# Performance work log

Measured on AMD Instinct MI355X. Metric: run time of the kernel, lower is better.

Reference implementation:

```python
import jax, jax.numpy as jnp
import numpy as np

DIM = 768
HEADS = 12
HID = 3072  # mlp_ratio * dim
BATCH = 8
FRAMES = 16
GRID = 14
NTOK = GRID * GRID
LN_EPS = 1e-5
EPS = 1e-6


def setup_inputs() -> dict:
    key = jax.random.key(0)
    ks = jax.random.split(key, 8)
    w = lambda k, shape: jax.random.normal(k, shape, jnp.float32) * 0.02
    return {
        "x": jax.random.normal(ks[0], (BATCH * FRAMES, NTOK, DIM), jnp.float32),
        "ln1_w": jnp.ones((DIM,), jnp.float32),
        "ln1_b": jnp.zeros((DIM,), jnp.float32),
        "qkv_w": w(ks[1], (3 * DIM, DIM)),
        "proj_w": w(ks[2], (DIM, DIM)),
        "proj_b": jnp.zeros((DIM,), jnp.float32),
        "ln2_w": jnp.ones((DIM,), jnp.float32),
        "ln2_b": jnp.zeros((DIM,), jnp.float32),
        "fc1_w": w(ks[3], (HID, DIM)),
        "fc1_b": jnp.zeros((HID,), jnp.float32),
        "dw_w": w(ks[4], (HID, 1, 3, 3)),
        "dw_b": jnp.zeros((HID,), jnp.float32),
        "fc2_w": w(ks[5], (DIM, HID)),
        "fc2_b": jnp.zeros((DIM,), jnp.float32),
        "H": GRID,
        "W": GRID,
        "num_frames": FRAMES,
    }


def _layernorm(x, w, b):
    mu = jnp.mean(x, axis=-1, keepdims=True)
    var = jnp.mean(jnp.square(x - mu), axis=-1, keepdims=True)
    return (x - mu) * jax.lax.rsqrt(var + LN_EPS) * w + b


def _joint_ts_attention(xn, qkv_w, proj_w, proj_b, num_frames):
    # xn: (b*f, n, c)
    Bt, n, C = xn.shape
    h = HEADS
    e = C // h
    scale = e ** (-0.5)
    qkv = jnp.einsum('bnc,dc->bnd', xn, qkv_w).reshape(Bt, n, 3, h, e)
    q, k, v = qkv[:, :, 0], qkv[:, :, 1], qkv[:, :, 2]
    # ReLU feature map + scale offset
    q_ = jax.nn.relu(q) + scale
    k_ = jax.nn.relu(k) + scale
    b = Bt // num_frames
    m = num_frames * n  # joint time-space sequence length
    q_ = q_.reshape(b, m, h, e)
    k_ = k_.reshape(b, m, h, e)
    v_ = v.reshape(b, m, h, e)
    # kv_: (b, h, e, e)
    kv = jnp.einsum('bnhe,bnhd->bhed', k_, v_)
    k_sum = jnp.sum(k_, axis=1)  # (b, h, e)
    z = 1.0 / (jnp.einsum('bnhe,bhe->bnh', q_, k_sum) + EPS)  # (b, m, h)
    out = jnp.einsum('bnhe,bhed->bnhd', q_, kv) * z[..., None]  # (b, m, h, e)
    out = out.reshape(Bt, n, C)
    return jnp.einsum('bnc,dc->bnd', out, proj_w) + proj_b


def _dwconv(x, w, b, H, W):
    # x: (B, N, C) -> NCHW depthwise 3x3, pad 1
    Bn, n, c = x.shape
    xi = jnp.transpose(x, (0, 2, 1)).reshape(Bn, c, H, W)
    y = jax.lax.conv_general_dilated(
        xi, w, window_strides=(1, 1), padding=((1, 1), (1, 1)),
        dimension_numbers=('NCHW', 'OIHW', 'NCHW'), feature_group_count=c)
    y = y + b[None, :, None, None]
    return jnp.transpose(y.reshape(Bn, c, n), (0, 2, 1))


def reference(x, ln1_w, ln1_b, qkv_w, proj_w, proj_b, ln2_w, ln2_b,
              fc1_w, fc1_b, dw_w, dw_b, fc2_w, fc2_b, H, W, num_frames):
    # x = x + attn(norm1(x), num_frames)
    x = x + _joint_ts_attention(_layernorm(x, ln1_w, ln1_b), qkv_w, proj_w, proj_b, num_frames)
    # x = x + mlp(norm2(x), H, W)
    xn = _layernorm(x, ln2_w, ln2_b)
    hdn = jnp.einsum('bnc,hc->bnh', xn, fc1_w) + fc1_b
    hdn = _dwconv(hdn, dw_w, dw_b, H, W)
    hdn = jax.nn.gelu(hdn, approximate=False)
    out = jnp.einsum('bnh,ch->bnc', hdn, fc2_w) + fc2_b
    return x + out
```

## Files before the change

### kernel.cpp

```cpp
#include <hip/hip_runtime.h>

typedef unsigned short u16;
typedef unsigned int u32;

typedef __bf16 bf16x8 __attribute__((ext_vector_type(8)));
typedef float f32x4 __attribute__((ext_vector_type(4)));

#define DIM 768
#define HID 3072
#define NTOK 196
#define BT 128
#define NTOKENS (BT * NTOK)
#define MJ 3136
#define HEADS 12

#define SZ_WB   ((size_t)(2304*768 + 768*768 + 3072*768 + 768*3072) * 2)
#define SZ_XN   ((size_t)NTOKENS * DIM * 2)
#define SZ_QKV  ((size_t)NTOKENS * 2304 * 2)
#define SZ_X2   ((size_t)NTOKENS * DIM * 4)
#define SZ_HDN  ((size_t)NTOKENS * HID * 2)
#define SZ_KV   ((size_t)96 * 4096 * 4)
#define SZ_KS   ((size_t)96 * 64 * 4)
#define WS_NEED (SZ_WB + SZ_XN + SZ_QKV + SZ_X2 + SZ_HDN + SZ_KV + SZ_KS)

static void* g_buf = nullptr;

__device__ __forceinline__ float b2f(u16 u) {
  union { u32 i; float f; } x; x.i = ((u32)u) << 16; return x.f;
}
__device__ __forceinline__ u16 f2b(float f) {
  u32 x = __float_as_uint(f);
  return (u16)((x + 0x7fffu + ((x >> 16) & 1u)) >> 16);
}

__device__ __forceinline__ void gload_lds16(const u16* g, u16* l) {
  __builtin_amdgcn_global_load_lds(
      (const __attribute__((address_space(1))) u32*)g,
      (__attribute__((address_space(3))) u32*)l, 16, 0, 0);
}

__global__ __launch_bounds__(256) void cvt_f32_bf16(const float* __restrict__ in,
    u16* __restrict__ out, int n4)
{
  int i = blockIdx.x * 256 + threadIdx.x;
  if (i < n4) {
    float4 f = ((const float4*)in)[i];
    ushort4 r;
    r.x = f2b(f.x); r.y = f2b(f.y); r.z = f2b(f.z); r.w = f2b(f.w);
    ((ushort4*)out)[i] = r;
  }
}

__global__ __launch_bounds__(256) void zero_f32(float* __restrict__ p, int n) {
  int i = blockIdx.x * 256 + threadIdx.x;
  if (i < n) p[i] = 0.0f;
}

__global__ __launch_bounds__(256) void ln_kernel(const float* __restrict__ xin,
    const float* __restrict__ w, const float* __restrict__ b, u16* __restrict__ out)
{
  const int token = blockIdx.x * 4 + (threadIdx.x >> 6);
  const int lane = threadIdx.x & 63;
  float v[12];
  const float* x = xin + (size_t)token * DIM;
#pragma unroll
  for (int c = 0; c < 3; ++c) {
    float4 f = *(const float4*)(x + c * 256 + lane * 4);
    v[c*4+0] = f.x; v[c*4+1] = f.y; v[c*4+2] = f.z; v[c*4+3] = f.w;
  }
  float s = 0.f, sq = 0.f;
#pragma unroll
  for (int i = 0; i < 12; ++i) { s += v[i]; sq += v[i] * v[i]; }
#pragma unroll
  for (int off = 32; off > 0; off >>= 1) {
    s += __shfl_xor(s, off, 64);
    sq += __shfl_xor(sq, off, 64);
  }
  const float mean = s * (1.0f / 768.0f);
  const float var = sq * (1.0f / 768.0f) - mean * mean;
  const float rstd = rsqrtf(var + 1e-5f);
  u16* o = out + (size_t)token * DIM;
#pragma unroll
  for (int c = 0; c < 3; ++c) {
    float4 wv = *(const float4*)(w + c * 256 + lane * 4);
    float4 bv = *(const float4*)(b + c * 256 + lane * 4);
    ushort4 r;
    r.x = f2b((v[c*4+0] - mean) * rstd * wv.x + bv.x);
    r.y = f2b((v[c*4+1] - mean) * rstd * wv.y + bv.y);
    r.z = f2b((v[c*4+2] - mean) * rstd * wv.z + bv.z);
    r.w = f2b((v[c*4+3] - mean) * rstd * wv.w + bv.w);
    *(ushort4*)(o + c * 256 + lane * 4) = r;
  }
}

template<int MODE, int NXT, int NN, int KK>
__global__ __launch_bounds__(512, 2) void gemm8(
    const u16* __restrict__ A, const u16* __restrict__ W,
    const float* __restrict__ bias, const float* __restrict__ res,
    void* __restrict__ out)
{
  extern __shared__ char smem[];
  u16* As = (u16*)smem;
  u16* Bs = (u16*)(smem + 65536);

  const int t = threadIdx.x;
  const int l = t & 63;
  const int w = t >> 6;
  const int wm = w >> 2;
  const int wn = w & 3;

  constexpr int TOTAL = 98 * NXT;
  constexpr int Q8 = TOTAL >> 3;
  constexpr int R8 = TOTAL & 7;
  const int orig = blockIdx.x;
  const int xcd = orig & 7;
  const int idx = orig >> 3;
  const int wg = (xcd < R8) ? (xcd * (Q8 + 1) + idx)
                            : (R8 * (Q8 + 1) + (xcd - R8) * Q8 + idx);
  const int m0 = (wg / NXT) * 256;
  const int n0 = (wg % NXT) * 256;

  const int srow = w * 16 + (l >> 3);
  const int scol = ((l & 7) ^ (l >> 3)) * 8;
  const u16* gA = A + (size_t)(m0 + srow) * KK + scol;
  const u16* gB = W + (size_t)(n0 + srow) * KK + scol;
  u16* lA = As + w * 1024;
  u16* lB = Bs + w * 1024;

#define STAGE_A(bb, h, kt) do { \
    const u16* g_ = gA + (size_t)(h) * 128 * KK + (size_t)(kt) * 64; \
    u16* l_ = lA + (bb) * 16384 + (h) * 8192; \
    gload_lds16(g_, l_); \
    gload_lds16(g_ + (size_t)8 * KK, l_ + 512); } while (0)
#define STAGE_B(bb, h, kt) do { \
    const u16* g_ = gB + (size_t)(h) * 128 * KK + (size_t)(kt) * 64; \
    u16* l_ = lB + (bb) * 16384 + (h) * 8192; \
    gload_lds16(g_, l_); \
    gload_lds16(g_ + (size_t)8 * KK, l_ + 512); } while (0)

  const int lm = l & 15;
  const int qq = l >> 4;
  const int acol = (qq << 4) ^ ((l & 7) << 4);
  const int abase = (wm * 128 + lm) * 128 + acol;
  const int bbase = (wn * 64 + lm) * 128 + acol;

  f32x4 acc[8][4];
#pragma unroll
  for (int mi = 0; mi < 8; ++mi)
#pragma unroll
    for (int ni = 0; ni < 4; ++ni) acc[mi][ni] = (f32x4){0.f, 0.f, 0.f, 0.f};

  constexpr int NT = KK / 64;

  STAGE_A(0, 0, 0); STAGE_A(0, 1, 0); STAGE_B(0, 0, 0); STAGE_B(0, 1, 0);
  STAGE_A(1, 0, 1);
  asm volatile("s_waitcnt vmcnt(2)" ::: "memory");
  __builtin_amdgcn_s_barrier();

  for (int ti = 0; ti < NT; ++ti) {
    const int cb = ti & 1, nb = cb ^ 1;
    const char* Ac = (const char*)As + cb * 32768;
    const char* Bc = (const char*)Bs + cb * 32768;
    bf16x8 am[4][2], b01[2][2], b23[2][2];

#pragma unroll
    for (int mi = 0; mi < 4; ++mi) {
      const int off = abase + mi * 2048;
      am[mi][0] = *(const bf16x8*)(Ac + off);
      am[mi][1] = *(const bf16x8*)(Ac + (off ^ 64));
    }
#pragma unroll
    for (int ni = 0; ni < 2; ++ni) {
      const int off = bbase + ni * 2048;
      b01[ni][0] = *(const bf16x8*)(Bc + off);
      b01[ni][1] = *(const bf16x8*)(Bc + (off ^ 64));
    }
    if (ti + 1 < NT) STAGE_A(nb, 1, ti + 1);
    asm volatile("" ::: "memory");
    __builtin_amdgcn_s_barrier();
    asm volatile("s_waitcnt lgkmcnt(0)" ::: "memory");
    __builtin_amdgcn_s_setprio(1);
#pragma unroll
    for (int mi = 0; mi < 4; ++mi)
#pragma unroll
      for (int ni = 0; ni < 2; ++ni) {
        acc[mi][ni] = __builtin_amdgcn_mfma_f32_16x16x32_bf16(am[mi][0], b01[ni][0], acc[mi][ni], 0, 0, 0);
        acc[mi][ni] = __builtin_amdgcn_mfma_f32_16x16x32_bf16(am[mi][1], b01[ni][1], acc[mi][ni], 0, 0, 0);
      }
    __builtin_amdgcn_s_setprio(0);
    asm volatile("" ::: "memory");
    __builtin_amdgcn_s_barrier();

#pragma unroll
    for (int ni = 0; ni < 2; ++ni) {
      const int off = bbase + (ni + 2) * 2048;
      b23[ni][0] = *(const bf16x8*)(Bc + off);
      b23[ni][1] = *(const bf16x8*)(Bc + (off ^ 64));
    }
    if (ti + 1 < NT) STAGE_B(nb, 0, ti + 1);
    asm volatile("" ::: "memory");
    __builtin_amdgcn_s_barrier();
    asm volatile("s_waitcnt lgkmcnt(0)" ::: "memory");
    __builtin_amdgcn_s_setprio(1);
#pragma unroll
    for (int mi = 0; mi < 4; ++mi)
#pragma unroll
      for (int ni = 0; ni < 2; ++ni) {
        acc[mi][ni + 2] = __builtin_amdgcn_mfma_f32_16x16x32_bf16(am[mi][0], b23[ni][0], acc[mi][ni + 2], 0, 0, 0);
        acc[mi][ni + 2] = __builtin_amdgcn_mfma_f32_16x16x32_bf16(am[mi][1], b23[ni][1], acc[mi][ni + 2], 0, 0, 0);
      }
    __builtin_amdgcn_s_setprio(0);
    asm volatile("" ::: "memory");
    __builtin_amdgcn_s_barrier();

#pragma unroll
    for (int mi = 0; mi < 4; ++mi) {
      const int off = abase + 8192 + mi * 2048;
      am[mi][0] = *(const bf16x8*)(Ac + off);
      am[mi][1] = *(const bf16x8*)(Ac + (off ^ 64));
    }
    if (ti + 1 < NT) STAGE_B(nb, 1, ti + 1);
    asm volatile("" ::: "memory");
    __builtin_amdgcn_s_barrier();
    asm volatile("s_waitcnt lgkmcnt(0)" ::: "memory");
    __builtin_amdgcn_s_setprio(1);
#pragma unroll
    for (int mi = 0; mi < 4; ++mi)
#pragma unroll
      for (int ni = 0; ni < 2; ++ni) {
        acc[mi + 4][ni + 2] = __builtin_amdgcn_mfma_f32_16x16x32_bf16(am[mi][0], b23[ni][0], acc[mi + 4][ni + 2], 0, 0, 0);
        acc[mi + 4][ni + 2] = __builtin_amdgcn_mfma_f32_16x16x32_bf16(am[mi][1], b23[ni][1], acc[mi + 4][ni + 2], 0, 0, 0);
      }
    __builtin_amdgcn_s_setprio(0);
    asm volatile("" ::: "memory");
    __builtin_amdgcn_s_barrier();

    if (ti + 2 < NT) {
      STAGE_A(cb, 0, ti + 2);
      asm volatile("s_waitcnt vmcnt(2)" ::: "memory");
    } else {
      asm volatile("s_waitcnt vmcnt(0)" ::: "memory");
    }
    __builtin_amdgcn_s_barrier();
    __builtin_amdgcn_s_setprio(1);
#pragma unroll
    for (int mi = 0; mi < 4; ++mi)
#pragma unroll
      for (int ni = 0; ni < 2; ++ni) {
        acc[mi + 4][ni] = __builtin_amdgcn_mfma_f32_16x16x32_bf16(am[mi][0], b01[ni][0], acc[mi + 4][ni], 0, 0, 0);
        acc[mi + 4][ni] = __builtin_amdgcn_mfma_f32_16x16x32_bf16(am[mi][1], b01[ni][1], acc[mi + 4][ni], 0, 0, 0);
      }
    __builtin_amdgcn_s_setprio(0);
    asm volatile("" ::: "memory");
    __builtin_amdgcn_s_barrier();
  }
#undef STAGE_A
#undef STAGE_B

#pragma unroll
  for (int mi = 0; mi < 8; ++mi) {
    const int rbase = m0 + wm * 128 + mi * 16 + qq * 4;
#pragma unroll
    for (int ni = 0; ni < 4; ++ni) {
      const int col = n0 + wn * 64 + ni * 16 + lm;
      float bv = 0.f;
      if (MODE != 0) bv = bias[col];
#pragma unroll
      for (int r = 0; r < 4; ++r) {
        float v = acc[mi][ni][r];
        const size_t idxo = (size_t)(rbase + r) * NN + col;
        if (MODE == 0) {
          if (col < 1536) v = fmaxf(v, 0.0f) + 0.125f;
          ((u16*)out)[idxo] = f2b(v);
        } else if (MODE == 1) {
          ((float*)out)[idxo] = v + bv + res[idxo];
        } else if (MODE == 2) {
          ((u16*)out)[idxo] = f2b(v + bv);
        } else {
          ((float*)out)[idxo] = v + bv + res[idxo];
        }
      }
    }
  }
}

__global__ __launch_bounds__(256) void kv_reduce(const u16* __restrict__ qkv,
    float* __restrict__ kv, float* __restrict__ ksum)
{
  const int bh = blockIdx.x;
  const int s = blockIdx.y;
  const int b = bh / 12, h = bh % 12;
  __shared__ __align__(16) u16 ks[64 * 64];
  __shared__ __align__(16) u16 vs[64 * 64];
  const int t = threadIdx.x;
  const int e = t & 63;
  const int dg = (t >> 6) * 16;

  float acc[16];
#pragma unroll
  for (int j = 0; j < 16; ++j) acc[j] = 0.f;
  float ksacc = 0.f;

  for (int ch = s; ch < 49; ch += 8) {
    const size_t tokbase = (size_t)b * MJ + ch * 64;
    __syncthreads();
#pragma unroll
    for (int i = 0; i < 2; ++i) {
      int c = t + i * 256;
      int row = c >> 3, eo = (c & 7) * 8;
      const u16* base = qkv + (tokbase + row) * 2304 + h * 64 + eo;
      *(uint4*)&ks[row * 64 + eo] = *(const uint4*)(base + 768);
      *(uint4*)&vs[row * 64 + eo] = *(const uint4*)(base + 1536);
    }
    __syncthreads();
    for (int m = 0; m < 64; ++m) {
      float kf = b2f(ks[m * 64 + e]);
      ksacc += kf;
      bf16x8 v0 = *(const bf16x8*)&vs[m * 64 + dg];
      bf16x8 v1 = *(const bf16x8*)&vs[m * 64 + dg + 8];
#pragma unroll
      for (int j = 0; j < 8; ++j) {
        acc[j]     += kf * (float)v0[j];
        acc[j + 8] += kf * (float)v1[j];
      }
    }
  }
  float* dst = kv + (size_t)bh * 4096 + e * 64 + dg;
#pragma unroll
  for (int j = 0; j < 16; ++j) atomicAdd(&dst[j], acc[j]);
  if (dg == 0) atomicAdd(&ksum[bh * 64 + e], ksacc);
}

__global__ __launch_bounds__(256) void attn_out(const u16* __restrict__ qkv,
    const float* __restrict__ kv, const float* __restrict__ ksum,
    u16* __restrict__ outp)
{
  const int chunk = blockIdx.x;
  const int h = blockIdx.y;
  const int b = blockIdx.z;
  __shared__ float kvs[4096];
  __shared__ float kss[64];
  __shared__ float qs[4096];
  const int t = threadIdx.x;
  const float* kvsrc = kv + (size_t)(b * 12 + h) * 4096;
  for (int i = t; i < 1024; i += 256)
    ((float4*)kvs)[i] = ((const float4*)kvsrc)[i];
  if (t < 64) kss[t] = ksum[(b * 12 + h) * 64 + t];
  __syncthreads();
  const int wv = t >> 6, lane = t & 63;
  float* qw = &qs[wv * 1024];
  const size_t tok0 = (size_t)b * MJ + chunk * 64 + wv * 16;
#pragma unroll
  for (int i = 0; i < 16; ++i) {
    float q = b2f(qkv[(tok0 + i) * 2304 + h * 64 + lane]);
    float pd = q * kss[lane];
#pragma unroll
    for (int off = 32; off > 0; off >>= 1) pd += __shfl_xor(pd, off, 64);
    qw[i * 64 + lane] = q * (1.0f / (pd + 1e-6f));
  }
  float o[16];
#pragma unroll
  for (int i = 0; i < 16; ++i) o[i] = 0.f;
  for (int e = 0; e < 64; ++e) {
    const float kvc = kvs[e * 64 + lane];
#pragma unroll
    for (int i = 0; i < 16; ++i) o[i] += qw[i * 64 + e] * kvc;
  }
#pragma unroll
  for (int i = 0; i < 16; ++i)
    outp[(tok0 + i) * 768 + h * 64 + lane] = f2b(o[i]);
}

__global__ __launch_bounds__(256) void dwconv_gelu(u16* __restrict__ hdn,
    const float* __restrict__ w, const float* __restrict__ bias)
{
  __shared__ u16 pl[196 * 64];
  const int cb = blockIdx.x;
  const int fr = blockIdx.y;
  const int t = threadIdx.x;
  const int c0 = cb * 64;
  u16* base = hdn + (size_t)fr * 196 * HID + c0;
  for (int i = 0; i < 49; ++i) {
    int idx = i * 256 + t;
    int p = idx >> 6, c = idx & 63;
    pl[idx] = base[(size_t)p * HID + c];
  }
  __syncthreads();
  const int c = t & 63;
  const int pg = t >> 6;
  float wr[9];
#pragma unroll
  for (int k = 0; k < 9; ++k) wr[k] = w[(c0 + c) * 9 + k];
  const float bv = bias[c0 + c];
  for (int j = 0; j < 49; ++j) {
    const int p = pg + j * 4;
    const int py = p / 14, px = p % 14;
    float a = bv;
#pragma unroll
    for (int ky = 0; ky < 3; ++ky) {
      int yy = py + ky - 1;
      if (yy < 0 || yy > 13) continue;
#pragma unroll
      for (int kx = 0; kx < 3; ++kx) {
        int xx = px + kx - 1;
        if (xx < 0 || xx > 13) continue;
        a += wr[ky * 3 + kx] * b2f(pl[(yy * 14 + xx) * 64 + c]);
      }
    }
    float g = 0.5f * a * (1.0f + erff(a * 0.70710678118654752f));
    base[(size_t)p * HID + c] = f2b(g);
  }
}

static void set_gemm_attrs() {
  (void)hipFuncSetAttribute(reinterpret_cast<const void*>(&gemm8<0, 9, 2304, 768>),
                            hipFuncAttributeMaxDynamicSharedMemorySize, 131072);
  (void)hipFuncSetAttribute(reinterpret_cast<const void*>(&gemm8<1, 3, 768, 768>),
                            hipFuncAttributeMaxDynamicSharedMemorySize, 131072);
  (void)hipFuncSetAttribute(reinterpret_cast<const void*>(&gemm8<2, 12, 3072, 768>),
                            hipFuncAttributeMaxDynamicSharedMemorySize, 131072);
  (void)hipFuncSetAttribute(reinterpret_cast<const void*>(&gemm8<3, 3, 768, 3072>),
                            hipFuncAttributeMaxDynamicSharedMemorySize, 131072);
}
struct WsInit {
  WsInit() {
    (void)hipMalloc(&g_buf, WS_NEED);
    set_gemm_attrs();
  }
};
static WsInit g_wsinit;

extern "C" void kernel_launch(void* const* d_in, const int* in_sizes, int n_in,
                              void* d_out, int out_size, void* d_ws, size_t ws_size,
                              hipStream_t stream)
{
  (void)in_sizes; (void)n_in; (void)out_size;
  static bool attrs_once = [] { set_gemm_attrs(); return true; }();
  (void)attrs_once;

  const float* x     = (const float*)d_in[0];
  const float* ln1w  = (const float*)d_in[1];
  const float* ln1b  = (const float*)d_in[2];
  const float* qkvw  = (const float*)d_in[3];
  const float* projw = (const float*)d_in[4];
  const float* projb = (const float*)d_in[5];
  const float* ln2w  = (const float*)d_in[6];
  const float* ln2b  = (const float*)d_in[7];
  const float* fc1w  = (const float*)d_in[8];
  const float* fc1b  = (const float*)d_in[9];
  const float* dww   = (const float*)d_in[10];
  const float* dwb   = (const float*)d_in[11];
  const float* fc2w  = (const float*)d_in[12];
  const float* fc2b  = (const float*)d_in[13];

  char* p = (ws_size >= WS_NEED) ? (char*)d_ws : (char*)g_buf;
  u16* WQKV  = (u16*)p;   p += (size_t)2304 * 768 * 2;
  u16* WPROJ = (u16*)p;   p += (size_t)768 * 768 * 2;
  u16* WFC1  = (u16*)p;   p += (size_t)3072 * 768 * 2;
  u16* WFC2  = (u16*)p;   p += (size_t)768 * 3072 * 2;
  u16* XN    = (u16*)p;   p += SZ_XN;
  u16* QKV   = (u16*)p;   p += SZ_QKV;
  float* X2  = (float*)p; p += SZ_X2;
  u16* HDN   = (u16*)p;   p += SZ_HDN;
  float* KV  = (float*)p; p += SZ_KV;
  float* KS  = (float*)p; p += SZ_KS;

  cvt_f32_bf16<<<(2304*768/4 + 255)/256, 256, 0, stream>>>(qkvw, WQKV, 2304*768/4);
  cvt_f32_bf16<<<(768*768/4 + 255)/256, 256, 0, stream>>>(projw, WPROJ, 768*768/4);
  cvt_f32_bf16<<<(3072*768/4 + 255)/256, 256, 0, stream>>>(fc1w, WFC1, 3072*768/4);
  cvt_f32_bf16<<<(768*3072/4 + 255)/256, 256, 0, stream>>>(fc2w, WFC2, 768*3072/4);

  const int nz = 96 * 4096 + 96 * 64;
  zero_f32<<<(nz + 255) / 256, 256, 0, stream>>>(KV, nz);
  ln_kernel<<<NTOKENS / 4, 256, 0, stream>>>(x, ln1w, ln1b, XN);
  gemm8<0, 9, 2304, 768><<<98 * 9, 512, 131072, stream>>>(XN, WQKV, nullptr, nullptr, QKV);
  kv_reduce<<<dim3(96, 8), 256, 0, stream>>>(QKV, KV, KS);
  attn_out<<<dim3(49, 12, 8), 256, 0, stream>>>(QKV, KV, KS, XN);
  gemm8<1, 3, 768, 768><<<98 * 3, 512, 131072, stream>>>(XN, WPROJ, projb, x, X2);
  ln_kernel<<<NTOKENS / 4, 256, 0, stream>>>(X2, ln2w, ln2b, QKV);
  gemm8<2, 12, 3072, 768><<<98 * 12, 512, 131072, stream>>>(QKV, WFC1, fc1b, nullptr, HDN);
  dwconv_gelu<<<dim3(48, 128), 256, 0, stream>>>(HDN, dww, dwb);
  gemm8<3, 3, 768, 3072><<<98 * 3, 512, 131072, stream>>>(HDN, WFC2, fc2b, X2, (float*)d_out);
}
```

Measured before the change: 1.114 ms.

## Reorder GEMM prefetch stages and vectorize depthwise conv with wider channel tiles

The GEMM main loop now issues both halves of the next A tile together, two iterations ahead, and spreads the B-tile prefetches over the first two compute phases, with the vmcnt waits adjusted to match. This is meant to issue global-to-LDS loads earlier and hide more latency. The dwconv+GELU kernel now covers 128 channels per block and loads with 16-byte vector reads into a padded LDS tile. Each thread computes 4 channels with ushort4 LDS reads and stores, which cuts the number of scalar 2-byte global accesses and halves the grid.

```diff
diff --git a/kernel.cpp b/kernel.cpp
--- a/kernel.cpp
+++ b/kernel.cpp
@@ -153,8 +153,8 @@
   constexpr int NT = KK / 64;
 
   STAGE_A(0, 0, 0); STAGE_A(0, 1, 0); STAGE_B(0, 0, 0); STAGE_B(0, 1, 0);
-  STAGE_A(1, 0, 1);
-  asm volatile("s_waitcnt vmcnt(2)" ::: "memory");
+  STAGE_A(1, 0, 1); STAGE_A(1, 1, 1);
+  asm volatile("s_waitcnt vmcnt(4)" ::: "memory");
   __builtin_amdgcn_s_barrier();
 
   for (int ti = 0; ti < NT; ++ti) {
@@ -175,7 +175,7 @@
       b01[ni][0] = *(const bf16x8*)(Bc + off);
       b01[ni][1] = *(const bf16x8*)(Bc + (off ^ 64));
     }
-    if (ti + 1 < NT) STAGE_A(nb, 1, ti + 1);
+    if (ti + 1 < NT) STAGE_B(nb, 0, ti + 1);
     asm volatile("" ::: "memory");
     __builtin_amdgcn_s_barrier();
     asm volatile("s_waitcnt lgkmcnt(0)" ::: "memory");
@@ -197,7 +197,7 @@
       b23[ni][0] = *(const bf16x8*)(Bc + off);
       b23[ni][1] = *(const bf16x8*)(Bc + (off ^ 64));
     }
-    if (ti + 1 < NT) STAGE_B(nb, 0, ti + 1);
+    if (ti + 1 < NT) STAGE_B(nb, 1, ti + 1);
     asm volatile("" ::: "memory");
     __builtin_amdgcn_s_barrier();
     asm volatile("s_waitcnt lgkmcnt(0)" ::: "memory");
@@ -219,7 +219,6 @@
       am[mi][0] = *(const bf16x8*)(Ac + off);
       am[mi][1] = *(const bf16x8*)(Ac + (off ^ 64));
     }
-    if (ti + 1 < NT) STAGE_B(nb, 1, ti + 1);
     asm volatile("" ::: "memory");
     __builtin_amdgcn_s_barrier();
     asm volatile("s_waitcnt lgkmcnt(0)" ::: "memory");
@@ -237,7 +236,8 @@
 
     if (ti + 2 < NT) {
       STAGE_A(cb, 0, ti + 2);
-      asm volatile("s_waitcnt vmcnt(2)" ::: "memory");
+      STAGE_A(cb, 1, ti + 2);
+      asm volatile("s_waitcnt vmcnt(4)" ::: "memory");
     } else {
       asm volatile("s_waitcnt vmcnt(0)" ::: "memory");
     }
@@ -374,28 +374,38 @@
 __global__ __launch_bounds__(256) void dwconv_gelu(u16* __restrict__ hdn,
     const float* __restrict__ w, const float* __restrict__ bias)
 {
-  __shared__ u16 pl[196 * 64];
+  __shared__ u16 pl[196 * 136];
   const int cb = blockIdx.x;
   const int fr = blockIdx.y;
   const int t = threadIdx.x;
-  const int c0 = cb * 64;
+  const int c0 = cb * 128;
   u16* base = hdn + (size_t)fr * 196 * HID + c0;
-  for (int i = 0; i < 49; ++i) {
+#pragma unroll
+  for (int i = 0; i < 13; ++i) {
     int idx = i * 256 + t;
-    int p = idx >> 6, c = idx & 63;
-    pl[idx] = base[(size_t)p * HID + c];
+    if (idx < 3136) {
+      int p = idx >> 4, cq = idx & 15;
+      *(uint4*)&pl[p * 136 + cq * 8] = *(const uint4*)(base + (size_t)p * HID + cq * 8);
+    }
   }
   __syncthreads();
-  const int c = t & 63;
-  const int pg = t >> 6;
-  float wr[9];
-#pragma unroll
-  for (int k = 0; k < 9; ++k) wr[k] = w[(c0 + c) * 9 + k];
-  const float bv = bias[c0 + c];
-  for (int j = 0; j < 49; ++j) {
-    const int p = pg + j * 4;
+  const int pc = t & 31;
+  const int pg = t >> 5;
+  const int cc = pc * 4;
+  float wr[36];
+#pragma unroll
+  for (int k = 0; k < 9; ++k)
+#pragma unroll
+    for (int u = 0; u < 4; ++u) wr[k * 4 + u] = w[(c0 + cc + u) * 9 + k];
+  float bv[4];
+#pragma unroll
+  for (int u = 0; u < 4; ++u) bv[u] = bias[c0 + cc + u];
+
+  for (int j = 0; j < 25; ++j) {
+    const int p = pg + j * 8;
+    if (p >= 196) break;
     const int py = p / 14, px = p % 14;
-    float a = bv;
+    float a0 = bv[0], a1 = bv[1], a2 = bv[2], a3 = bv[3];
 #pragma unroll
     for (int ky = 0; ky < 3; ++ky) {
       int yy = py + ky - 1;
@@ -404,11 +414,20 @@
       for (int kx = 0; kx < 3; ++kx) {
         int xx = px + kx - 1;
         if (xx < 0 || xx > 13) continue;
-        a += wr[ky * 3 + kx] * b2f(pl[(yy * 14 + xx) * 64 + c]);
-      }
-    }
-    float g = 0.5f * a * (1.0f + erff(a * 0.70710678118654752f));
-    base[(size_t)p * HID + c] = f2b(g);
+        ushort4 tv = *(const ushort4*)&pl[(yy * 14 + xx) * 136 + cc];
+        const float* wk = &wr[(ky * 3 + kx) * 4];
+        a0 += wk[0] * b2f(tv.x);
+        a1 += wk[1] * b2f(tv.y);
+        a2 += wk[2] * b2f(tv.z);
+        a3 += wk[3] * b2f(tv.w);
+      }
+    }
+    ushort4 r;
+    r.x = f2b(0.5f * a0 * (1.0f + erff(a0 * 0.70710678118654752f)));
+    r.y = f2b(0.5f * a1 * (1.0f + erff(a1 * 0.70710678118654752f)));
+    r.z = f2b(0.5f * a2 * (1.0f + erff(a2 * 0.70710678118654752f)));
+    r.w = f2b(0.5f * a3 * (1.0f + erff(a3 * 0.70710678118654752f)));
+    *(ushort4*)(base + (size_t)p * HID + cc) = r;
   }
 }
 
@@ -479,6 +498,6 @@
   gemm8<1, 3, 768, 768><<<98 * 3, 512, 131072, stream>>>(XN, WPROJ, projb, x, X2);
   ln_kernel<<<NTOKENS / 4, 256, 0, stream>>>(X2, ln2w, ln2b, QKV);
   gemm8<2, 12, 3072, 768><<<98 * 12, 512, 131072, stream>>>(QKV, WFC1, fc1b, nullptr, HDN);
-  dwconv_gelu<<<dim3(48, 128), 256, 0, stream>>>(HDN, dww, dwb);
+  dwconv_gelu<<<dim3(24, 128), 256, 0, stream>>>(HDN, dww, dwb);
   gemm8<3, 3, 768, 3072><<<98 * 3, 512, 131072, stream>>>(HDN, WFC2, fc2b, X2, (float*)d_out);
 }
```

Measured after the change: 1.084 ms. 1.03x faster.
